# Optimization experiments

Hardware: AMD Instinct MI355X
Metric: run time of the kernel (lower is better)

The kernel has to match this reference:

```python
import jax, jax.numpy as jnp
import numpy as np

NUM_FRAMES = 8
HEAD_DIM = 32


def setup_inputs() -> dict:
    key = jax.random.key(0)
    k1, k2, k3, k4, k5 = jax.random.split(key, 5)
    dim = 384
    nh = dim // HEAD_DIM
    return {
        "x": jax.random.normal(k1, (16, dim, 16, 16), dtype=jnp.float32),
        "qk_w": jax.random.normal(k2, (2 * dim, dim), dtype=jnp.float32) * 0.02,
        "alpha": jax.random.normal(k3, (1, nh, 1, 1), dtype=jnp.float32),
        "beta": jax.random.normal(k4, (1, nh, 1, 1), dtype=jnp.float32),
        "gamma": jax.random.normal(k5, (1, nh, 1, 1), dtype=jnp.float32),
    }


def reference(x, qk_w, alpha, beta, gamma):
    B_T, C, H, W = x.shape
    B = B_T // NUM_FRAMES
    N = NUM_FRAMES * H * W
    nh = C // HEAD_DIM
    scale = HEAD_DIM ** -0.5

    # [B*T,C,H,W] -> [B,N,C] tokens (frames-major token order, matching torch)
    xt = x.reshape(B, NUM_FRAMES, C, H, W).transpose(0, 2, 1, 3, 4)  # B,C,T,H,W
    xt = xt.reshape(B, C, N).transpose(0, 2, 1)                      # B,N,C

    qk = (xt @ qk_w.T).reshape(B, N, 2, nh, HEAD_DIM)
    qk = qk.transpose(2, 0, 3, 1, 4)                                 # 2,B,nh,N,hd
    q, k = qk[0], qk[1]
    v = xt.reshape(B, N, nh, HEAD_DIM).transpose(0, 2, 1, 3)         # B,nh,N,hd

    attn = jax.nn.softmax(jnp.einsum('bhnd,bhmd->bhnm', q * scale, k), axis=-1)
    eye = jnp.eye(N, dtype=x.dtype)
    Cm = jnp.full((N, N), 1.0 / N, dtype=x.dtype)
    attn = alpha * eye + beta * attn - gamma * Cm                    # B,nh,N,N

    out = jnp.einsum('bhnm,bhmd->bhnd', attn, v)
    out = out.transpose(0, 2, 1, 3).reshape(B, N, C)                 # B,N,C
    out = out.transpose(0, 2, 1).reshape(B, C, NUM_FRAMES, H, W)
    out = out.transpose(0, 2, 1, 3, 4).reshape(B_T, C, H, W)
    return out
```

## Files before the change

kernel.cpp:

```cpp
#include <hip/hip_runtime.h>
#include <hip/hip_bf16.h>

typedef __attribute__((ext_vector_type(8))) short short8;
typedef __attribute__((ext_vector_type(4))) float f32x4;
typedef __attribute__((ext_vector_type(2))) float f32x2;
typedef __attribute__((ext_vector_type(16))) float f32x16;
typedef __attribute__((ext_vector_type(4))) unsigned int uint4v;
typedef unsigned short ushort_t;
typedef unsigned int uint_t;

#define NFRAMES 8
#define HD 32
#define CDIM 384
#define NH 12
#define NTOK 2048
#define QKCOLS 768
#define TILEB 2048
#define QSCALE 0.2550541213313367f

static __device__ __forceinline__ ushort_t f2bf(float f) {
    __hip_bfloat16 h = __float2bfloat16(f);
    return *reinterpret_cast<ushort_t*>(&h);
}
static __device__ __forceinline__ uint_t packbf2(float lo, float hi) {
    return (uint_t)f2bf(lo) | ((uint_t)f2bf(hi) << 16);
}

__global__ __launch_bounds__(256) void pack_kernel(const float* __restrict__ x,
                                                   const float* __restrict__ qk_w,
                                                   ushort_t* __restrict__ Xt,
                                                   ushort_t* __restrict__ VFG,
                                                   float* __restrict__ psum,
                                                   ushort_t* __restrict__ Wb) {
    int tid = threadIdx.x;
    int bid = blockIdx.x;
    if (bid >= 192) {
        int vid = (bid - 192) * 256 + tid;
        int j = vid / 48;
        float scale = (j < CDIM) ? QSCALE : 1.0f;
        const float* src = qk_w + vid * 8;
        float4 a = *(const float4*)src;
        float4 b = *(const float4*)(src + 4);
        uint4 o = make_uint4(packbf2(a.x * scale, a.y * scale), packbf2(a.z * scale, a.w * scale),
                             packbf2(b.x * scale, b.y * scale), packbf2(b.z * scale, b.w * scale));
        *(uint4*)(Wb + vid * 8) = o;
        return;
    }
    __shared__ float lds[32 * 256];
    __shared__ float red[8][32];
    int bt = bid & 15;
    int h = bid >> 4;
    int c0 = h * 32;
    const float* src = x + ((long)bt * CDIM + c0) * 256;
#pragma unroll
    for (int i = 0; i < 32; ++i) lds[i * 256 + tid] = src[i * 256 + tid];
    __syncthreads();
    int b = bt >> 3, t = bt & 7;
    long n = (long)b * NTOK + t * 256 + tid;
    uint4* dst = reinterpret_cast<uint4*>(Xt + n * CDIM + c0);
#pragma unroll
    for (int k = 0; k < 4; ++k) {
        uint_t vv[4];
#pragma unroll
        for (int q = 0; q < 4; ++q)
            vv[q] = packbf2(lds[(k * 8 + q * 2) * 256 + tid], lds[(k * 8 + q * 2 + 1) * 256 + tid]);
        dst[k] = make_uint4(vv[0], vv[1], vv[2], vv[3]);
    }
    int bh = b * NH + h;
#pragma unroll
    for (int pass = 0; pass < 4; ++pass) {
        int kt = pass * 2 + (tid >> 7);
        int slot = tid & 127;
        int d = slot & 31, c2 = slot >> 5;
        const float* p0 = &lds[d * 256 + kt * 32 + c2 * 8];
        float4 a = *(const float4*)p0;
        float4 bb = *(const float4*)(p0 + 4);
        uint4 o = make_uint4(packbf2(a.x, a.y), packbf2(a.z, a.w),
                             packbf2(bb.x, bb.y), packbf2(bb.z, bb.w));
        *(uint4*)((char*)VFG + ((size_t)(bh * 64 + t * 8 + kt)) * TILEB + slot * 16) = o;
    }
    int ch = tid & 31, seg = tid >> 5;
    float s = 0.f;
#pragma unroll
    for (int j = 0; j < 32; ++j) s += lds[ch * 256 + seg * 32 + j];
    red[seg][ch] = s;
    __syncthreads();
    if (tid < 32) {
        float tot = 0.f;
#pragma unroll
        for (int i = 0; i < 8; ++i) tot += red[i][tid];
        psum[(bt * NH + h) * HD + tid] = tot;
    }
}

__global__ __launch_bounds__(256) void proj_kernel(const ushort_t* __restrict__ Xt,
                                                   const ushort_t* __restrict__ Wb,
                                                   ushort_t* __restrict__ QFG,
                                                   ushort_t* __restrict__ KFG) {
    __shared__ __align__(16) ushort_t tb[4][32][40];
    int tid = threadIdx.x;
    int lane = tid & 63;
    int w = tid >> 6;
    int wid = blockIdx.x * 4 + w;
    int mb = wid / 24, nb = wid % 24;
    int j31 = lane & 31, hi = lane >> 5;
    const char* Arow = (const char*)(Xt + (mb * 32 + j31) * CDIM + hi * 8);
    const char* Brow = (const char*)(Wb + (nb * 32 + j31) * CDIM + hi * 8);
    f32x16 acc = {};
#pragma unroll
    for (int k16 = 0; k16 < 24; ++k16) {
        short8 a = *(const short8*)(Arow + k16 * 32);
        short8 bb = *(const short8*)(Brow + k16 * 32);
        acc = __builtin_amdgcn_mfma_f32_32x32x16_bf16(a, bb, acc, 0, 0, 0);
    }
#pragma unroll
    for (int q = 0; q < 16; ++q) {
        int row = (q & 3) + 8 * (q >> 2) + 4 * hi;
        tb[w][row][j31] = f2bf(acc[q]);
    }
    short8 f0 = *(const short8*)&tb[w][j31][hi * 8];
    short8 f1 = *(const short8*)&tb[w][j31][16 + hi * 8];
    int bsel = mb >> 6;
    int tile = mb & 63;
    int hh = (nb < 12) ? nb : nb - 12;
    ushort_t* dstbuf = (nb < 12) ? QFG : KFG;
    char* base = (char*)dstbuf + ((size_t)((bsel * NH + hh) * 64 + tile)) * TILEB;
    *(short8*)(base + lane * 16) = f0;
    *(short8*)(base + 1024 + lane * 16) = f1;
}

__global__ __launch_bounds__(256) void attn_kernel(
    const ushort_t* __restrict__ QFG, const ushort_t* __restrict__ KFG,
    const ushort_t* __restrict__ VFG, const float* __restrict__ x,
    const float* __restrict__ psum, const float* __restrict__ alpha,
    const float* __restrict__ beta, const float* __restrict__ gamma,
    float* __restrict__ out) {
    __shared__ float mrg[3 * 1088 + 32];

    int tid = threadIdx.x, lane = tid & 63, w = tid >> 6;
    int bid = blockIdx.x;
    int L = (bid & 7) * 192 + (bid >> 3);
    int rb = L & 63, bh = L >> 6;
    int h = bh % NH, b = bh / NH;
    int j31 = lane & 31, hi = lane >> 5;
    int qb = rb * 32;

    const char* Qb = (const char*)QFG + ((size_t)(bh * 64 + rb)) * TILEB;
    short8 qf0 = *(const short8*)(Qb + lane * 16);
    short8 qf1 = *(const short8*)(Qb + 1024 + lane * 16);

    const char* Kbase = (const char*)KFG + ((size_t)(bh * 64 + w * 16)) * TILEB + lane * 16;
    const char* Vbase = (const char*)VFG + ((size_t)(bh * 64 + w * 16)) * TILEB + lane * 16;

    f32x16 acc = {};
    f32x2 lp2 = {};

    short8 kA0, kA1, vA0, vA1, kB0, kB1, vB0, vB1;

#define LOADT(i, K0, K1, V0, V1)                              \
    {                                                         \
        size_t off = (size_t)(i)*TILEB;                       \
        K0 = *(const short8*)(Kbase + off);                   \
        K1 = *(const short8*)(Kbase + off + 1024);            \
        V0 = *(const short8*)(Vbase + off);                   \
        V1 = *(const short8*)(Vbase + off + 1024);            \
    }

#define COMPUTE(K0, K1, V0, V1)                                                    \
    {                                                                              \
        f32x16 s = {};                                                             \
        s = __builtin_amdgcn_mfma_f32_32x32x16_bf16(K0, qf0, s, 0, 0, 0);          \
        s = __builtin_amdgcn_mfma_f32_32x32x16_bf16(K1, qf1, s, 0, 0, 0);          \
        uint_t pk[8];                                                              \
        _Pragma("unroll")                                                          \
        for (int j = 0; j < 8; ++j) {                                              \
            float e0 = __builtin_amdgcn_exp2f(s[2 * j]);                           \
            float e1 = __builtin_amdgcn_exp2f(s[2 * j + 1]);                       \
            uint_t u0 = __builtin_bit_cast(uint_t, e0) + 0x8000u;                  \
            uint_t u1 = __builtin_bit_cast(uint_t, e1) + 0x8000u;                  \
            pk[j] = __builtin_amdgcn_perm(u1, u0, 0x07060302u);                    \
            f32x2 ee;                                                              \
            ee[0] = e0;                                                            \
            ee[1] = e1;                                                            \
            lp2 += ee;                                                             \
        }                                                                          \
        _Pragma("unroll")                                                          \
        for (int kh = 0; kh < 2; ++kh) {                                           \
            uint_t o0 = pk[kh * 4], o1 = pk[kh * 4 + 1];                           \
            uint_t o2 = pk[kh * 4 + 2], o3 = pk[kh * 4 + 3];                       \
            auto r02 = __builtin_amdgcn_permlane32_swap(o2, o0, false, false);     \
            auto r13 = __builtin_amdgcn_permlane32_swap(o3, o1, false, false);     \
            uint4v uu;                                                             \
            uu[0] = r02[1];                                  \
            uu[1] = r13[1];                                  \
            uu[2] = r02[0];                                  \
            uu[3] = r13[0];                                  \
            short8 pa = __builtin_bit_cast(short8, uu);                            \
            acc = __builtin_amdgcn_mfma_f32_32x32x16_bf16(pa, (kh ? V1 : V0), acc, 0, 0, 0); \
        }                                                                          \
    }

    LOADT(0, kA0, kA1, vA0, vA1);
#pragma unroll
    for (int i2 = 0; i2 < 8; ++i2) {
        int i = i2 * 2;
        if (i + 1 < 16) LOADT(i + 1, kB0, kB1, vB0, vB1);
        COMPUTE(kA0, kA1, vA0, vA1);
        if (i + 2 < 16) LOADT(i + 2, kA0, kA1, vA0, vA1);
        COMPUTE(kB0, kB1, vB0, vB1);
    }
#undef LOADT
#undef COMPUTE

    float lp = lp2[0] + lp2[1];

    if (w) {
        float* ab = mrg + (w - 1) * 1088;
#pragma unroll
        for (int q = 0; q < 16; ++q) ab[lane * 17 + q] = acc[q];
        ab[lane * 17 + 16] = lp;
    }
    __syncthreads();
    if (w == 0) {
#pragma unroll
        for (int q = 0; q < 16; ++q)
            acc[q] += mrg[lane * 17 + q] + mrg[1088 + lane * 17 + q] + mrg[2176 + lane * 17 + q];
        float lsum = lp + mrg[lane * 17 + 16] + mrg[1088 + lane * 17 + 16] + mrg[2176 + lane * 17 + 16];
        lsum += __shfl_xor(lsum, 32);
        float* Lb = mrg + 3 * 1088;
        if (!hi) Lb[j31] = lsum;
        float alpha_h = alpha[h], beta_h = beta[h], gamma_h = gamma[h];
        int d = j31, c = h * HD + d;
        float sv = 0.f;
#pragma unroll
        for (int t = 0; t < NFRAMES; ++t) sv += psum[((b * NFRAMES + t) * NH + h) * HD + d];
        float gsv = gamma_h * sv * (1.0f / NTOK);
#pragma unroll
        for (int q = 0; q < 16; ++q) {
            int qrow = (q & 3) + 8 * (q >> 2) + 4 * hi;
            int n = qb + qrow;
            float linv = 1.0f / Lb[qrow];
            long xidx = ((long)(b * NFRAMES + (n >> 8)) * CDIM + c) * 256 + (n & 255);
            out[xidx] = beta_h * acc[q] * linv + alpha_h * x[xidx] - gsv;
        }
    }
}

extern "C" void kernel_launch(void* const* d_in, const int* in_sizes, int n_in,
                              void* d_out, int out_size, void* d_ws, size_t ws_size,
                              hipStream_t stream) {
    const float* x = (const float*)d_in[0];
    const float* qk_w = (const float*)d_in[1];
    const float* alpha = (const float*)d_in[2];
    const float* beta = (const float*)d_in[3];
    const float* gamma = (const float*)d_in[4];
    float* out = (float*)d_out;

    char* ws = (char*)d_ws;
    ushort_t* Xt = (ushort_t*)ws;
    ushort_t* Wb = (ushort_t*)(ws + 3145728);
    ushort_t* QFG = (ushort_t*)(ws + 3735552);
    ushort_t* KFG = (ushort_t*)(ws + 6881280);
    ushort_t* VFG = (ushort_t*)(ws + 10027008);
    float* psum = (float*)(ws + 13172736);

    hipLaunchKernelGGL(pack_kernel, dim3(336), dim3(256), 0, stream, x, qk_w, Xt, VFG, psum, Wb);
    hipLaunchKernelGGL(proj_kernel, dim3(768), dim3(256), 0, stream, Xt, Wb, QFG, KFG);
    hipLaunchKernelGGL(attn_kernel, dim3(1536), dim3(256), 0, stream,
                       QFG, KFG, VFG, x, psum, alpha, beta, gamma, out);
}
```

Baseline: 56.54 us.

## Pad transpose LDS, simplify attention loop with setprio and hardware bf16 convert

The prep kernel's LDS tile is padded to a stride of 257 to avoid bank conflicts on the transposed reads, and its vector float4 LDS loads become scalar loads. The attention kernel drops the manual double-buffered K/V prefetch for a plain unrolled loop and adds s_setprio around the MFMAs. It also replaces the bit-trick bf16 rounding with v_cvt_pk_bf16_f32 and raises launch bounds to 8 waves per SIMD to force higher occupancy. Removing the explicit prefetch and capping registers may expose global-load latency, and the inline asm limits how freely the compiler can schedule.

Result: slower. 103.8 us (+83.6%).

```diff
diff --git a/kernel.cpp b/kernel.cpp
--- a/kernel.cpp
+++ b/kernel.cpp
@@ -2,7 +2,6 @@
 #include <hip/hip_bf16.h>
 
 typedef __attribute__((ext_vector_type(8))) short short8;
-typedef __attribute__((ext_vector_type(4))) float f32x4;
 typedef __attribute__((ext_vector_type(2))) float f32x2;
 typedef __attribute__((ext_vector_type(16))) float f32x16;
 typedef __attribute__((ext_vector_type(4))) unsigned int uint4v;
@@ -46,14 +45,14 @@
         *(uint4*)(Wb + vid * 8) = o;
         return;
     }
-    __shared__ float lds[32 * 256];
+    __shared__ float lds[32 * 257];
     __shared__ float red[8][32];
     int bt = bid & 15;
     int h = bid >> 4;
     int c0 = h * 32;
     const float* src = x + ((long)bt * CDIM + c0) * 256;
 #pragma unroll
-    for (int i = 0; i < 32; ++i) lds[i * 256 + tid] = src[i * 256 + tid];
+    for (int i = 0; i < 32; ++i) lds[i * 257 + tid] = src[i * 256 + tid];
     __syncthreads();
     int b = bt >> 3, t = bt & 7;
     long n = (long)b * NTOK + t * 256 + tid;
@@ -63,7 +62,7 @@
         uint_t vv[4];
 #pragma unroll
         for (int q = 0; q < 4; ++q)
-            vv[q] = packbf2(lds[(k * 8 + q * 2) * 256 + tid], lds[(k * 8 + q * 2 + 1) * 256 + tid]);
+            vv[q] = packbf2(lds[(k * 8 + q * 2) * 257 + tid], lds[(k * 8 + q * 2 + 1) * 257 + tid]);
         dst[k] = make_uint4(vv[0], vv[1], vv[2], vv[3]);
     }
     int bh = b * NH + h;
@@ -72,17 +71,15 @@
         int kt = pass * 2 + (tid >> 7);
         int slot = tid & 127;
         int d = slot & 31, c2 = slot >> 5;
-        const float* p0 = &lds[d * 256 + kt * 32 + c2 * 8];
-        float4 a = *(const float4*)p0;
-        float4 bb = *(const float4*)(p0 + 4);
-        uint4 o = make_uint4(packbf2(a.x, a.y), packbf2(a.z, a.w),
-                             packbf2(bb.x, bb.y), packbf2(bb.z, bb.w));
+        const float* p0 = &lds[d * 257 + kt * 32 + c2 * 8];
+        uint4 o = make_uint4(packbf2(p0[0], p0[1]), packbf2(p0[2], p0[3]),
+                             packbf2(p0[4], p0[5]), packbf2(p0[6], p0[7]));
         *(uint4*)((char*)VFG + ((size_t)(bh * 64 + t * 8 + kt)) * TILEB + slot * 16) = o;
     }
     int ch = tid & 31, seg = tid >> 5;
     float s = 0.f;
 #pragma unroll
-    for (int j = 0; j < 32; ++j) s += lds[ch * 256 + seg * 32 + j];
+    for (int j = 0; j < 32; ++j) s += lds[ch * 257 + seg * 32 + j];
     red[seg][ch] = s;
     __syncthreads();
     if (tid < 32) {
@@ -129,7 +126,7 @@
     *(short8*)(base + 1024 + lane * 16) = f1;
 }
 
-__global__ __launch_bounds__(256) void attn_kernel(
+__global__ __launch_bounds__(256, 8) void attn_kernel(
     const ushort_t* __restrict__ QFG, const ushort_t* __restrict__ KFG,
     const ushort_t* __restrict__ VFG, const float* __restrict__ x,
     const float* __restrict__ psum, const float* __restrict__ alpha,
@@ -155,62 +152,46 @@
     f32x16 acc = {};
     f32x2 lp2 = {};
 
-    short8 kA0, kA1, vA0, vA1, kB0, kB1, vB0, vB1;
-
-#define LOADT(i, K0, K1, V0, V1)                              \
-    {                                                         \
-        size_t off = (size_t)(i)*TILEB;                       \
-        K0 = *(const short8*)(Kbase + off);                   \
-        K1 = *(const short8*)(Kbase + off + 1024);            \
-        V0 = *(const short8*)(Vbase + off);                   \
-        V1 = *(const short8*)(Vbase + off + 1024);            \
-    }
-
-#define COMPUTE(K0, K1, V0, V1)                                                    \
-    {                                                                              \
-        f32x16 s = {};                                                             \
-        s = __builtin_amdgcn_mfma_f32_32x32x16_bf16(K0, qf0, s, 0, 0, 0);          \
-        s = __builtin_amdgcn_mfma_f32_32x32x16_bf16(K1, qf1, s, 0, 0, 0);          \
-        uint_t pk[8];                                                              \
-        _Pragma("unroll")                                                          \
-        for (int j = 0; j < 8; ++j) {                                              \
-            float e0 = __builtin_amdgcn_exp2f(s[2 * j]);                           \
-            float e1 = __builtin_amdgcn_exp2f(s[2 * j + 1]);                       \
-            uint_t u0 = __builtin_bit_cast(uint_t, e0) + 0x8000u;                  \
-            uint_t u1 = __builtin_bit_cast(uint_t, e1) + 0x8000u;                  \
-            pk[j] = __builtin_amdgcn_perm(u1, u0, 0x07060302u);                    \
-            f32x2 ee;                                                              \
-            ee[0] = e0;                                                            \
-            ee[1] = e1;                                                            \
-            lp2 += ee;                                                             \
-        }                                                                          \
-        _Pragma("unroll")                                                          \
-        for (int kh = 0; kh < 2; ++kh) {                                           \
-            uint_t o0 = pk[kh * 4], o1 = pk[kh * 4 + 1];                           \
-            uint_t o2 = pk[kh * 4 + 2], o3 = pk[kh * 4 + 3];                       \
-            auto r02 = __builtin_amdgcn_permlane32_swap(o2, o0, false, false);     \
-            auto r13 = __builtin_amdgcn_permlane32_swap(o3, o1, false, false);     \
-            uint4v uu;                                                             \
-            uu[0] = r02[1];                                  \
-            uu[1] = r13[1];                                  \
-            uu[2] = r02[0];                                  \
-            uu[3] = r13[0];                                  \
-            short8 pa = __builtin_bit_cast(short8, uu);                            \
-            acc = __builtin_amdgcn_mfma_f32_32x32x16_bf16(pa, (kh ? V1 : V0), acc, 0, 0, 0); \
-        }                                                                          \
-    }
-
-    LOADT(0, kA0, kA1, vA0, vA1);
-#pragma unroll
-    for (int i2 = 0; i2 < 8; ++i2) {
-        int i = i2 * 2;
-        if (i + 1 < 16) LOADT(i + 1, kB0, kB1, vB0, vB1);
-        COMPUTE(kA0, kA1, vA0, vA1);
-        if (i + 2 < 16) LOADT(i + 2, kA0, kA1, vA0, vA1);
-        COMPUTE(kB0, kB1, vB0, vB1);
-    }
-#undef LOADT
-#undef COMPUTE
+#pragma unroll
+    for (int i = 0; i < 16; ++i) {
+        size_t off = (size_t)i * TILEB;
+        short8 K0 = *(const short8*)(Kbase + off);
+        short8 K1 = *(const short8*)(Kbase + off + 1024);
+        f32x16 s = {};
+        __builtin_amdgcn_s_setprio(1);
+        s = __builtin_amdgcn_mfma_f32_32x32x16_bf16(K0, qf0, s, 0, 0, 0);
+        s = __builtin_amdgcn_mfma_f32_32x32x16_bf16(K1, qf1, s, 0, 0, 0);
+        __builtin_amdgcn_s_setprio(0);
+        short8 V0 = *(const short8*)(Vbase + off);
+        short8 V1 = *(const short8*)(Vbase + off + 1024);
+        uint_t pk[8];
+#pragma unroll
+        for (int j = 0; j < 8; ++j) {
+            float e0 = __builtin_amdgcn_exp2f(s[2 * j]);
+            float e1 = __builtin_amdgcn_exp2f(s[2 * j + 1]);
+            f32x2 ee;
+            ee[0] = e0;
+            ee[1] = e1;
+            lp2 += ee;
+            asm("v_cvt_pk_bf16_f32 %0, %1, %2" : "=v"(pk[j]) : "v"(e0), "v"(e1));
+        }
+#pragma unroll
+        for (int kh = 0; kh < 2; ++kh) {
+            uint_t o0 = pk[kh * 4], o1 = pk[kh * 4 + 1];
+            uint_t o2 = pk[kh * 4 + 2], o3 = pk[kh * 4 + 3];
+            auto r02 = __builtin_amdgcn_permlane32_swap(o2, o0, false, false);
+            auto r13 = __builtin_amdgcn_permlane32_swap(o3, o1, false, false);
+            uint4v uu;
+            uu[0] = r02[1];
+            uu[1] = r13[1];
+            uu[2] = r02[0];
+            uu[3] = r13[0];
+            short8 pa = __builtin_bit_cast(short8, uu);
+            __builtin_amdgcn_s_setprio(1);
+            acc = __builtin_amdgcn_mfma_f32_32x32x16_bf16(pa, (kh ? V1 : V0), acc, 0, 0, 0);
+            __builtin_amdgcn_s_setprio(0);
+        }
+    }
 
     float lp = lp2[0] + lp2[1];
 
```
